# Kernel tuning notes

Measured on AMD Instinct MI355X. Metric: run time of the kernel, lower is better.

## Reference

```python
import jax, jax.numpy as jnp
import numpy as np

B, S, HID = 1, 4096, 2048
H, KVH, D = 16, 8, 128
EPS = 1e-6
SCALE = D ** -0.5


def rms_norm(x, w):
    # normalize over last axis in float32, per-head weight of size D
    xf = x.astype(jnp.float32)
    var = jnp.mean(xf * xf, axis=-1, keepdims=True)
    return (w * xf * jax.lax.rsqrt(var + EPS)).astype(x.dtype)


def rotate_half(x):
    x1, x2 = jnp.split(x, 2, axis=-1)
    return jnp.concatenate([-x2, x1], axis=-1)


def setup_inputs() -> dict:
    key = jax.random.key(0)
    ks = jax.random.split(key, 12)
    x = jax.random.normal(ks[0], (B, S, HID), jnp.float32)
    # RoPE tables
    inv_freq = 1.0 / (10000.0 ** (jnp.arange(0, D, 2, dtype=jnp.float32) / D))
    t = jnp.arange(S, dtype=jnp.float32)
    freqs = jnp.outer(t, inv_freq)                       # [S, D/2]
    emb = jnp.concatenate([freqs, freqs], axis=-1)       # [S, D]
    cos, sin = jnp.cos(emb), jnp.sin(emb)
    # causal additive mask
    neg = jnp.finfo(jnp.float32).min
    mask = jnp.where(jnp.tril(jnp.ones((S, S), bool)), 0.0, neg)[None, None]
    sc = 0.02
    Wq = jax.random.normal(ks[1], (H * D, HID), jnp.float32) * sc
    bq = jnp.zeros((H * D,), jnp.float32)
    Wk = jax.random.normal(ks[2], (KVH * D, HID), jnp.float32) * sc
    bk = jnp.zeros((KVH * D,), jnp.float32)
    Wv = jax.random.normal(ks[3], (KVH * D, HID), jnp.float32) * sc
    bv = jnp.zeros((KVH * D,), jnp.float32)
    Wo = jax.random.normal(ks[4], (HID, H * D), jnp.float32) * sc
    qn_w = jnp.ones((D,), jnp.float32)
    kn_w = jnp.ones((D,), jnp.float32)
    return {"x": x, "cos": cos, "sin": sin, "mask": mask,
            "Wq": Wq, "bq": bq, "Wk": Wk, "bk": bk, "Wv": Wv, "bv": bv,
            "Wo": Wo, "qn_w": qn_w, "kn_w": kn_w}


def reference(x, cos, sin, mask, Wq, bq, Wk, bk, Wv, bv, Wo, qn_w, kn_w):
    b, s, _ = x.shape
    q = (x @ Wq.T + bq).reshape(b, s, H, D)
    k = (x @ Wk.T + bk).reshape(b, s, KVH, D)
    v = (x @ Wv.T + bv).reshape(b, s, KVH, D)
    q = rms_norm(q, qn_w)
    k = rms_norm(k, kn_w)
    # RoPE: cos/sin [S, D] broadcast over batch and head dims
    c = cos[None, :, None, :]
    sn = sin[None, :, None, :]
    q = q * c + rotate_half(q) * sn
    k = k * c + rotate_half(k) * sn
    # GQA: repeat kv heads (repeat_interleave along head axis)
    reps = H // KVH
    k = jnp.repeat(k, reps, axis=2)
    v = jnp.repeat(v, reps, axis=2)
    # [b, H, s, d]
    q = q.transpose(0, 2, 1, 3)
    k = k.transpose(0, 2, 1, 3)
    v = v.transpose(0, 2, 1, 3)
    scores = jnp.einsum('bhqd,bhkd->bhqk', q, k) * SCALE + mask
    attn = jax.nn.softmax(scores.astype(jnp.float32), axis=-1).astype(q.dtype)
    out = jnp.einsum('bhqk,bhkd->bhqd', attn, v)
    out = out.transpose(0, 2, 1, 3).reshape(b, s, H * D)
    return out @ Wo.T
```

## Files before the change

kernel.cpp:

```cpp
#include <hip/hip_runtime.h>
#include <hip/hip_bf16.h>
#include <stdint.h>

#define S_LEN 4096
#define HID 2048
#define NH 16
#define KVH 8
#define DH 128
#define EPS 1e-6f
#define SCALE 0.08838834764831845f
#define LOG2E 1.4426950408889634f

#if __has_builtin(__builtin_amdgcn_exp2f)
#define EXP2(x) __builtin_amdgcn_exp2f(x)
#else
#define EXP2(x) exp2f(x)
#endif

typedef __bf16 bf16x8 __attribute__((ext_vector_type(8)));
typedef __bf16 bf16x4 __attribute__((ext_vector_type(4)));
typedef float f32x4 __attribute__((ext_vector_type(4)));

__device__ inline void gl_lds16(const __bf16* g, __bf16* l) {
  __builtin_amdgcn_global_load_lds(
      (const __attribute__((address_space(1))) void*)g,
      (__attribute__((address_space(3))) void*)l, 16, 0, 0);
}

__global__ __launch_bounds__(256) void f2b4(
    const float* __restrict__ in, __bf16* __restrict__ out, int n4) {
  int i = blockIdx.x * 256 + threadIdx.x;
  if (i < n4) {
    float4 v = ((const float4*)in)[i];
    bf16x4 o;
    o[0] = (__bf16)v.x; o[1] = (__bf16)v.y; o[2] = (__bf16)v.z; o[3] = (__bf16)v.w;
    ((bf16x4*)out)[i] = o;
  }
}

template <typename TC>
__global__ __launch_bounds__(256) void gemm128(
    const __bf16* __restrict__ A, const __bf16* __restrict__ B,
    const float* __restrict__ bias, TC* __restrict__ C,
    int N, int K, int bias_mode)
{
  __shared__ __attribute__((aligned(16))) __bf16 As[128 * 32];
  __shared__ __attribute__((aligned(16))) __bf16 Bs[128 * 32];
  const int wave = threadIdx.x >> 6, lane = threadIdx.x & 63;
  const int quad = lane >> 4, l16 = lane & 15;
  const int wm = wave >> 1, wn = wave & 1;
  const int m0 = blockIdx.y * 128, n0 = blockIdx.x * 128;
  const int srow = lane >> 2, scol = (lane & 3) * 8;

  f32x4 acc[4][4] = {};

  for (int k0 = 0; k0 < K; k0 += 32) {
    __syncthreads();
#pragma unroll
    for (int j = wave; j < 8; j += 4) {
      gl_lds16(A + (size_t)(m0 + j * 16 + srow) * K + k0 + scol, As + j * 512);
      gl_lds16(B + (size_t)(n0 + j * 16 + srow) * K + k0 + scol, Bs + j * 512);
    }
    __syncthreads();
    bf16x8 af[4], bfr[4];
#pragma unroll
    for (int s = 0; s < 4; ++s) {
      af[s]  = *(const bf16x8*)(As + (wm * 64 + s * 16 + l16) * 32 + quad * 8);
      bfr[s] = *(const bf16x8*)(Bs + (wn * 64 + s * 16 + l16) * 32 + quad * 8);
    }
#pragma unroll
    for (int ms = 0; ms < 4; ++ms)
#pragma unroll
      for (int ns = 0; ns < 4; ++ns)
        acc[ms][ns] = __builtin_amdgcn_mfma_f32_16x16x32_bf16(
            af[ms], bfr[ns], acc[ms][ns], 0, 0, 0);
  }

#pragma unroll
  for (int ms = 0; ms < 4; ++ms)
#pragma unroll
    for (int ns = 0; ns < 4; ++ns)
#pragma unroll
      for (int r = 0; r < 4; ++r) {
        int row = m0 + wm * 64 + ms * 16 + quad * 4 + r;
        int col = n0 + wn * 64 + ns * 16 + l16;
        float v = acc[ms][ns][r];
        if (bias_mode == 1) v += bias[col];
        else if (bias_mode == 2) v += bias[row];
        C[(size_t)row * N + col] = (TC)v;
      }
}

__global__ __launch_bounds__(256) void rmsnorm_rope(
    __bf16* __restrict__ q, __bf16* __restrict__ k,
    const float* __restrict__ cosb, const float* __restrict__ sinb,
    const float* __restrict__ qw, const float* __restrict__ kw)
{
  const int wave = threadIdx.x >> 6;
  const int lane = threadIdx.x & 63;
  const int row = blockIdx.x * 4 + wave;
  const int s   = row / (NH + KVH);
  const int idx = row % (NH + KVH);

  __bf16* base;
  const float* w;
  float oscale;
  if (idx < NH) { base = q + ((size_t)s * NH + idx) * DH;         w = qw; oscale = SCALE * LOG2E; }
  else          { base = k + ((size_t)s * KVH + (idx - NH)) * DH; w = kw; oscale = 1.0f; }

  float x1 = (float)base[lane];
  float x2 = (float)base[lane + 64];
  float ss = x1 * x1 + x2 * x2;
#pragma unroll
  for (int m = 1; m < 64; m <<= 1) ss += __shfl_xor(ss, m, 64);
  float inv = rsqrtf(ss * (1.0f / 128.0f) + EPS);

  float xh1 = x1 * inv * w[lane];
  float xh2 = x2 * inv * w[lane + 64];
  const float* cs = cosb + (size_t)s * DH;
  const float* sn = sinb + (size_t)s * DH;
  base[lane]      = (__bf16)((xh1 * cs[lane]      - xh2 * sn[lane])      * oscale);
  base[lane + 64] = (__bf16)((xh2 * cs[lane + 64] + xh1 * sn[lane + 64]) * oscale);
}

__global__ __launch_bounds__(256) void attn2(
    const __bf16* __restrict__ q,
    const __bf16* __restrict__ k,
    const __bf16* __restrict__ vt,
    __bf16* __restrict__ o)
{
  __shared__ __attribute__((aligned(16))) __bf16 Ks[2][64 * DH];
  __shared__ __attribute__((aligned(16))) __bf16 Vs[2][DH * 64];
  __shared__ __attribute__((aligned(16))) __bf16 pl[4][16 * 72];
  const int wave = threadIdx.x >> 6, lane = threadIdx.x & 63;
  const int quad = lane >> 4, l16 = lane & 15;
  const int h = blockIdx.y, kvh = h >> 1;

  const __bf16* kh = k + (size_t)kvh * DH;
  const __bf16* vh = vt + (size_t)kvh * DH * S_LEN;

  int krow[4], kcol[4], vrow[4], vcol[4];
#pragma unroll
  for (int i = 0; i < 4; ++i) {
    int j = wave + i * 4;
    int r = j * 4 + (lane >> 4);
    int cbK = ((lane & 15) * 16) ^ ((r & 7) << 4);
    krow[i] = r; kcol[i] = cbK >> 1;
    int d = j * 8 + (lane >> 3);
    int cbV = ((lane & 7) * 16) ^ ((d & 7) << 4);
    vrow[i] = d; vcol[i] = cbV >> 1;
  }
  auto stage = [&](int buf, int k0) {
#pragma unroll
    for (int i = 0; i < 4; ++i)
      gl_lds16(kh + (size_t)(k0 + krow[i]) * (KVH * DH) + kcol[i],
               &Ks[buf][(wave + i * 4) * 512]);
#pragma unroll
    for (int i = 0; i < 4; ++i)
      gl_lds16(vh + (size_t)vrow[i] * S_LEN + k0 + vcol[i],
               &Vs[buf][(wave + i * 4) * 512]);
  };

  for (int phase = 0; phase < 2; ++phase) {
    const int qt = phase == 0 ? (int)blockIdx.x : 63 - (int)blockIdx.x;
    const int qbase = qt * 64 + wave * 16;

    bf16x8 qa[4];
    const __bf16* qrow = q + ((size_t)(qbase + l16) * NH + h) * DH + quad * 8;
#pragma unroll
    for (int c = 0; c < 4; ++c) qa[c] = *(const bf16x8*)(qrow + c * 32);

    f32x4 oacc[8] = {};
    float mrun[4], lrun[4];
#pragma unroll
    for (int r = 0; r < 4; ++r) { mrun[r] = -3.0e38f; lrun[r] = 0.0f; }

    __syncthreads();
    stage(0, 0);

    for (int kt = 0; kt <= qt; ++kt) {
      const int cur = kt & 1;
      const int k0 = kt * 64;
      __syncthreads();
      if (kt < qt) stage(cur ^ 1, k0 + 64);

      const char* ksb = (const char*)Ks[cur];
      const char* vsb = (const char*)Vs[cur];

      f32x4 sc[4] = {};
#pragma unroll
      for (int tt = 0; tt < 4; ++tt) {
        const int row = tt * 16 + l16;
        const int swz = (row & 7) << 4;
#pragma unroll
        for (int c = 0; c < 4; ++c) {
          bf16x8 bk = *(const bf16x8*)(ksb + row * 256 + ((c * 64 + quad * 16) ^ swz));
          sc[tt] = __builtin_amdgcn_mfma_f32_16x16x32_bf16(qa[c], bk, sc[tt], 0, 0, 0);
        }
      }
      if (kt == qt) {
#pragma unroll
        for (int tt = 0; tt < 4; ++tt)
#pragma unroll
          for (int r = 0; r < 4; ++r) {
            int col = k0 + tt * 16 + l16;
            int row = qbase + quad * 4 + r;
            if (col > row) sc[tt][r] = -3.0e38f;
          }
      }
      float pmax[4];
      bool defer = true;
#pragma unroll
      for (int r = 0; r < 4; ++r) {
        float mx = fmaxf(fmaxf(sc[0][r], sc[1][r]), fmaxf(sc[2][r], sc[3][r]));
        pmax[r] = mx;
        defer = defer && (mx - mrun[r] <= 8.0f);
      }
      if (__all(defer)) {
#pragma unroll
        for (int r = 0; r < 4; ++r) {
          float s0 = EXP2(sc[0][r] - mrun[r]);
          float s1 = EXP2(sc[1][r] - mrun[r]);
          float s2 = EXP2(sc[2][r] - mrun[r]);
          float s3 = EXP2(sc[3][r] - mrun[r]);
          sc[0][r] = s0; sc[1][r] = s1; sc[2][r] = s2; sc[3][r] = s3;
          lrun[r] += (s0 + s1) + (s2 + s3);
        }
      } else {
#pragma unroll
        for (int r = 0; r < 4; ++r) {
          float mx = pmax[r];
#pragma unroll
          for (int msk = 1; msk < 16; msk <<= 1) mx = fmaxf(mx, __shfl_xor(mx, msk, 64));
          float mnew = fmaxf(mrun[r], mx);
          float sum = 0.0f;
#pragma unroll
          for (int tt = 0; tt < 4; ++tt) {
            float p = EXP2(sc[tt][r] - mnew);
            sc[tt][r] = p;
            sum += p;
          }
          float alpha = EXP2(mrun[r] - mnew);
          lrun[r] = lrun[r] * alpha + sum;
          mrun[r] = mnew;
#pragma unroll
          for (int c = 0; c < 8; ++c) oacc[c][r] *= alpha;
        }
      }
#pragma unroll
      for (int tt = 0; tt < 4; ++tt)
#pragma unroll
        for (int r = 0; r < 4; ++r)
          pl[wave][(quad * 4 + r) * 72 + tt * 16 + l16] = (__bf16)sc[tt][r];
      bf16x8 pa[2];
#pragma unroll
      for (int kc = 0; kc < 2; ++kc)
        pa[kc] = *(const bf16x8*)(pl[wave] + l16 * 72 + kc * 32 + quad * 8);
#pragma unroll
      for (int c = 0; c < 8; ++c)
#pragma unroll
        for (int kc = 0; kc < 2; ++kc) {
          const int d = c * 16 + l16;
          bf16x8 bv = *(const bf16x8*)(
              vsb + d * 128 + ((kc * 64 + quad * 16) ^ ((d & 7) << 4)));
          oacc[c] = __builtin_amdgcn_mfma_f32_16x16x32_bf16(pa[kc], bv, oacc[c], 0, 0, 0);
        }
    }

#pragma unroll
    for (int r = 0; r < 4; ++r) {
#pragma unroll
      for (int msk = 1; msk < 16; msk <<= 1) lrun[r] += __shfl_xor(lrun[r], msk, 64);
      lrun[r] = 1.0f / lrun[r];
    }
#pragma unroll
    for (int c = 0; c < 8; ++c)
#pragma unroll
      for (int r = 0; r < 4; ++r) {
        int row = qbase + quad * 4 + r;
        o[((size_t)row * NH + h) * DH + c * 16 + l16] = (__bf16)(oacc[c][r] * lrun[r]);
      }
  }
}

extern "C" void kernel_launch(void* const* d_in, const int* in_sizes, int n_in,
                              void* d_out, int out_size, void* d_ws, size_t ws_size,
                              hipStream_t stream) {
  const float* x    = (const float*)d_in[0];
  const float* cosb = (const float*)d_in[1];
  const float* sinb = (const float*)d_in[2];
  const float* Wq  = (const float*)d_in[4];
  const float* bq  = (const float*)d_in[5];
  const float* Wk  = (const float*)d_in[6];
  const float* bk  = (const float*)d_in[7];
  const float* Wv  = (const float*)d_in[8];
  const float* bv  = (const float*)d_in[9];
  const float* Wo  = (const float*)d_in[10];
  const float* qnw = (const float*)d_in[11];
  const float* knw = (const float*)d_in[12];
  float* out = (float*)d_out;

  char* ws = (char*)d_ws;
  __bf16* xb    = (__bf16*)(ws);
  __bf16* Wqb   = (__bf16*)(ws + (16u << 20));
  __bf16* Wkb   = (__bf16*)(ws + (24u << 20));
  __bf16* Wvb   = (__bf16*)(ws + (28u << 20));
  __bf16* kbuf  = (__bf16*)(ws + (32u << 20));
  __bf16* vtbuf = (__bf16*)(ws + (40u << 20));
  __bf16* Wob   = (__bf16*)(ws + (16u << 20));
  __bf16* ao    = (__bf16*)(ws);
  __bf16* qbuf = (__bf16*)d_out;

  dim3 blk(256);
  f2b4<<<dim3(8192), blk, 0, stream>>>(x,  xb,  2097152);
  f2b4<<<dim3(4096), blk, 0, stream>>>(Wq, Wqb, 1048576);
  f2b4<<<dim3(2048), blk, 0, stream>>>(Wk, Wkb, 524288);
  f2b4<<<dim3(2048), blk, 0, stream>>>(Wv, Wvb, 524288);
  gemm128<__bf16><<<dim3(16, 32), blk, 0, stream>>>(xb, Wqb, bq, qbuf, HID, HID, 1);
  gemm128<__bf16><<<dim3(8, 32), blk, 0, stream>>>(xb, Wkb, bk, kbuf, KVH * DH, HID, 1);
  gemm128<__bf16><<<dim3(32, 8), blk, 0, stream>>>(Wvb, xb, bv, vtbuf, S_LEN, HID, 2);
  rmsnorm_rope<<<dim3(S_LEN * (NH + KVH) / 4), blk, 0, stream>>>(
      qbuf, kbuf, cosb, sinb, qnw, knw);
  f2b4<<<dim3(4096), blk, 0, stream>>>(Wo, Wob, 1048576);
  attn2<<<dim3(32, NH), blk, 0, stream>>>(qbuf, kbuf, vtbuf, ao);
  gemm128<float><<<dim3(16, 32), blk, 0, stream>>>(ao, Wob, nullptr, out, HID, HID, 0);
}
```

Baseline: 541.7 us.

## Double-buffer GEMM LDS tiles and fuse Q and K projections into one launch

The GEMM kernel now uses two LDS buffers, issuing the next k-tile's global-to-LDS loads before computing on the current one, with one barrier per iteration instead of two. The Q and K projection GEMMs are merged into a single launch over 3072 output columns, relying on Wk's bf16 copy sitting right after Wq's. The epilogue routes columns to either output with separate bias and leading dimension. This aims to hide load latency and fill the GPU better, at the cost of more LDS per block and a per-element branch in the store.

```diff
diff --git a/kernel.cpp b/kernel.cpp
--- a/kernel.cpp
+++ b/kernel.cpp
@@ -42,31 +42,40 @@
 __global__ __launch_bounds__(256) void gemm128(
     const __bf16* __restrict__ A, const __bf16* __restrict__ B,
     const float* __restrict__ bias, TC* __restrict__ C,
-    int N, int K, int bias_mode)
+    int N, int K, int bias_mode, int ldc,
+    TC* __restrict__ C2, const float* __restrict__ bias2,
+    int nsplit, int ldc2)
 {
-  __shared__ __attribute__((aligned(16))) __bf16 As[128 * 32];
-  __shared__ __attribute__((aligned(16))) __bf16 Bs[128 * 32];
+  __shared__ __attribute__((aligned(16))) __bf16 As[2][128 * 32];
+  __shared__ __attribute__((aligned(16))) __bf16 Bs[2][128 * 32];
   const int wave = threadIdx.x >> 6, lane = threadIdx.x & 63;
   const int quad = lane >> 4, l16 = lane & 15;
   const int wm = wave >> 1, wn = wave & 1;
   const int m0 = blockIdx.y * 128, n0 = blockIdx.x * 128;
   const int srow = lane >> 2, scol = (lane & 3) * 8;
 
+  auto stage = [&](int buf, int k0) {
+#pragma unroll
+    for (int j = wave; j < 8; j += 4) {
+      gl_lds16(A + (size_t)(m0 + j * 16 + srow) * K + k0 + scol, &As[buf][j * 512]);
+      gl_lds16(B + (size_t)(n0 + j * 16 + srow) * K + k0 + scol, &Bs[buf][j * 512]);
+    }
+  };
+
   f32x4 acc[4][4] = {};
-
-  for (int k0 = 0; k0 < K; k0 += 32) {
+  const int nk = K >> 5;
+  stage(0, 0);
+
+  for (int kt = 0; kt < nk; ++kt) {
+    const int cur = kt & 1;
     __syncthreads();
-#pragma unroll
-    for (int j = wave; j < 8; j += 4) {
-      gl_lds16(A + (size_t)(m0 + j * 16 + srow) * K + k0 + scol, As + j * 512);
-      gl_lds16(B + (size_t)(n0 + j * 16 + srow) * K + k0 + scol, Bs + j * 512);
-    }
-    __syncthreads();
+    if (kt + 1 < nk) stage(cur ^ 1, (kt + 1) * 32);
+
     bf16x8 af[4], bfr[4];
 #pragma unroll
     for (int s = 0; s < 4; ++s) {
-      af[s]  = *(const bf16x8*)(As + (wm * 64 + s * 16 + l16) * 32 + quad * 8);
-      bfr[s] = *(const bf16x8*)(Bs + (wn * 64 + s * 16 + l16) * 32 + quad * 8);
+      af[s]  = *(const bf16x8*)(&As[cur][(wm * 64 + s * 16 + l16) * 32 + quad * 8]);
+      bfr[s] = *(const bf16x8*)(&Bs[cur][(wn * 64 + s * 16 + l16) * 32 + quad * 8]);
     }
 #pragma unroll
     for (int ms = 0; ms < 4; ++ms)
@@ -85,9 +94,10 @@
         int row = m0 + wm * 64 + ms * 16 + quad * 4 + r;
         int col = n0 + wn * 64 + ns * 16 + l16;
         float v = acc[ms][ns][r];
-        if (bias_mode == 1) v += bias[col];
+        if (bias_mode == 1) v += (col < nsplit) ? bias[col] : bias2[col - nsplit];
         else if (bias_mode == 2) v += bias[row];
-        C[(size_t)row * N + col] = (TC)v;
+        if (col < nsplit) C[(size_t)row * ldc + col] = (TC)v;
+        else              C2[(size_t)row * ldc2 + (col - nsplit)] = (TC)v;
       }
 }
 
@@ -316,12 +326,14 @@
   f2b4<<<dim3(4096), blk, 0, stream>>>(Wq, Wqb, 1048576);
   f2b4<<<dim3(2048), blk, 0, stream>>>(Wk, Wkb, 524288);
   f2b4<<<dim3(2048), blk, 0, stream>>>(Wv, Wvb, 524288);
-  gemm128<__bf16><<<dim3(16, 32), blk, 0, stream>>>(xb, Wqb, bq, qbuf, HID, HID, 1);
-  gemm128<__bf16><<<dim3(8, 32), blk, 0, stream>>>(xb, Wkb, bk, kbuf, KVH * DH, HID, 1);
-  gemm128<__bf16><<<dim3(32, 8), blk, 0, stream>>>(Wvb, xb, bv, vtbuf, S_LEN, HID, 2);
+  gemm128<__bf16><<<dim3(24, 32), blk, 0, stream>>>(
+      xb, Wqb, bq, qbuf, 3072, HID, 1, HID, kbuf, bk, HID, KVH * DH);
+  gemm128<__bf16><<<dim3(32, 8), blk, 0, stream>>>(
+      Wvb, xb, bv, vtbuf, S_LEN, HID, 2, S_LEN, nullptr, nullptr, S_LEN, 0);
   rmsnorm_rope<<<dim3(S_LEN * (NH + KVH) / 4), blk, 0, stream>>>(
       qbuf, kbuf, cosb, sinb, qnw, knw);
   f2b4<<<dim3(4096), blk, 0, stream>>>(Wo, Wob, 1048576);
   attn2<<<dim3(32, NH), blk, 0, stream>>>(qbuf, kbuf, vtbuf, ao);
-  gemm128<float><<<dim3(16, 32), blk, 0, stream>>>(ao, Wob, nullptr, out, HID, HID, 0);
-}
+  gemm128<float><<<dim3(16, 32), blk, 0, stream>>>(
+      ao, Wob, nullptr, out, HID, HID, 0, HID, nullptr, nullptr, HID, 0);
+}
```

After: 516.3 us. 4.7% less time.
